# Kernel optimization log

Measured on AMD Instinct MI355X. Metric: run time of the kernel, lower is better.

Reference implementation:

```python
import jax, jax.numpy as jnp
import numpy as np


def setup_inputs() -> dict:
    key = jax.random.key(0)
    # [B, C=3, T, H, W] raw video clips
    batch_x = jax.random.normal(key, (16, 3, 600, 72, 72), dtype=jnp.float32)
    return {"batch_x": batch_x}


def reference(batch_x):
    # Spatial mean over H, W -> RGB traces  [B, 3, N]
    x = jnp.mean(batch_x, axis=(3, 4))
    # First left singular vector of each 3xN trace matrix.
    # torch.svd(X) reduced -> U is [3, 3]; batched over B here.
    U, _, _ = jnp.linalg.svd(x, full_matrices=False)  # U: [B, 3, 3]
    S = U[..., 0]  # [B, 3] dominant left singular vector
    # Orthogonal projection P = I - S S^T (sign of S is irrelevant)
    P = jnp.eye(3, dtype=x.dtype) - jnp.einsum('bi,bj->bij', S, S)  # [B, 3, 3]
    Y = jnp.einsum('bij,bjn->bin', P, x)  # [B, 3, N]
    # Original takes channel index 1 (green) of projected signal
    return Y[:, 1, :]  # [B, N]
```

## Files before the change

kernel.cpp:

```cpp
#include <hip/hip_runtime.h>
#include <math.h>

#define HW_ELEMS 5184
#define HW_VEC   1296
#define NT       600
#define NC       3
#define NB       16
#define NSLABS   (NB * NC * NT)
#define MEAN_GRID 2048

__global__ __launch_bounds__(256) void mean_kernel(const float* __restrict__ in,
                                                   float* __restrict__ xbar) {
    const int lane   = threadIdx.x & 63;
    const int gwave  = (blockIdx.x * 256 + threadIdx.x) >> 6;
    const int nwaves = (MEAN_GRID * 256) >> 6;

    for (int slab = gwave; slab < NSLABS; slab += nwaves) {
        const float4* __restrict__ p =
            (const float4*)(in + (size_t)slab * HW_ELEMS);

        float s0 = 0.f, s1 = 0.f;
        #pragma unroll
        for (int i = 0; i < 20; i += 2) {
            float4 a = p[(i << 6) + lane];
            float4 b = p[((i + 1) << 6) + lane];
            s0 += (a.x + a.y) + (a.z + a.w);
            s1 += (b.x + b.y) + (b.z + b.w);
        }
        if (lane < 16) {
            float4 v = p[1280 + lane];
            s0 += (v.x + v.y) + (v.z + v.w);
        }
        float s = s0 + s1;

        #pragma unroll
        for (int off = 32; off; off >>= 1)
            s += __shfl_xor(s, off, 64);

        if (lane == 0) xbar[slab] = s * (1.0f / (float)HW_ELEMS);
    }
}

__global__ __launch_bounds__(256) void project_kernel(const float* __restrict__ xbar,
                                                      float* __restrict__ out) {
    const int b = blockIdx.x;
    __shared__ float  sx[NC][NT];
    __shared__ double red[6][256];
    __shared__ float  S[3];

    const float* xb = xbar + b * (NC * NT);
    for (int i = threadIdx.x; i < NC * NT; i += 256)
        ((float*)sx)[i] = xb[i];
    __syncthreads();

    double g0 = 0, g1 = 0, g2 = 0, g3 = 0, g4 = 0, g5 = 0;
    for (int t = threadIdx.x; t < NT; t += 256) {
        double x0 = (double)sx[0][t];
        double x1 = (double)sx[1][t];
        double x2 = (double)sx[2][t];
        g0 += x0 * x0; g1 += x0 * x1; g2 += x0 * x2;
        g3 += x1 * x1; g4 += x1 * x2; g5 += x2 * x2;
    }
    red[0][threadIdx.x] = g0; red[1][threadIdx.x] = g1; red[2][threadIdx.x] = g2;
    red[3][threadIdx.x] = g3; red[4][threadIdx.x] = g4; red[5][threadIdx.x] = g5;
    __syncthreads();
    for (int s = 128; s > 0; s >>= 1) {
        if (threadIdx.x < s) {
            #pragma unroll
            for (int k = 0; k < 6; k++)
                red[k][threadIdx.x] += red[k][threadIdx.x + s];
        }
        __syncthreads();
    }

    if (threadIdx.x == 0) {
        double M[3][3] = {{red[0][0], red[1][0], red[2][0]},
                          {red[1][0], red[3][0], red[4][0]},
                          {red[2][0], red[4][0], red[5][0]}};
        for (int it = 0; it < 40; it++) {
            double tr = M[0][0] + M[1][1] + M[2][2];
            double inv = (tr > 0.0) ? (1.0 / tr) : 1.0;
            double T[3][3];
            #pragma unroll
            for (int i = 0; i < 3; i++)
                #pragma unroll
                for (int j = 0; j < 3; j++) T[i][j] = M[i][j] * inv;
            #pragma unroll
            for (int i = 0; i < 3; i++)
                #pragma unroll
                for (int j = 0; j < 3; j++) {
                    double acc = 0.0;
                    #pragma unroll
                    for (int k = 0; k < 3; k++) acc += T[i][k] * T[k][j];
                    M[i][j] = acc;
                }
        }
        int jm = 0;
        if (M[1][1] > M[jm][jm]) jm = 1;
        if (M[2][2] > M[jm][jm]) jm = 2;
        double v0 = M[0][jm], v1 = M[1][jm], v2 = M[2][jm];
        double nrm = sqrt(v0 * v0 + v1 * v1 + v2 * v2);
        double inv = (nrm > 0.0) ? (1.0 / nrm) : 0.0;
        S[0] = (float)(v0 * inv);
        S[1] = (float)(v1 * inv);
        S[2] = (float)(v2 * inv);
    }
    __syncthreads();

    const float s0 = S[0], s1 = S[1], s2 = S[2];
    for (int t = threadIdx.x; t < NT; t += 256) {
        float x0 = sx[0][t], x1 = sx[1][t], x2 = sx[2][t];
        float d = s0 * x0 + s1 * x1 + s2 * x2;
        out[b * NT + t] = x1 - s1 * d;
    }
}

extern "C" void kernel_launch(void* const* d_in, const int* in_sizes, int n_in,
                              void* d_out, int out_size, void* d_ws, size_t ws_size,
                              hipStream_t stream) {
    const float* batch_x = (const float*)d_in[0];
    float* out  = (float*)d_out;
    float* xbar = (float*)d_ws;

    mean_kernel<<<MEAN_GRID, 256, 0, stream>>>(batch_x, xbar);
    project_kernel<<<NB, 256, 0, stream>>>(xbar, out);
}
```

Before: 752.7 us.

## Fuse mean and projection kernels via last-block atomic counter per batch

Merges the spatial-mean and projection kernels into a single launch. Each 256-thread block reduces four slabs, one per wave, using nontemporal vector loads. The last block to finish for a batch, found with a global atomic counter, computes the Gram matrix, dominant vector and projection. This removes a kernel launch and the serial tail of the small projection kernel. In exchange it adds atomics, thread fences, and a counter that must be reset for the next call.

```diff
diff --git a/kernel.cpp b/kernel.cpp
--- a/kernel.cpp
+++ b/kernel.cpp
@@ -2,48 +2,56 @@
 #include <math.h>
 
 #define HW_ELEMS 5184
-#define HW_VEC   1296
 #define NT       600
 #define NC       3
 #define NB       16
 #define NSLABS   (NB * NC * NT)
-#define MEAN_GRID 2048
+#define SLABS_PER_BLOCK 4
+#define NBLOCKS  (NSLABS / SLABS_PER_BLOCK)
+#define BLOCKS_PER_BATCH (NBLOCKS / NB)
 
-__global__ __launch_bounds__(256) void mean_kernel(const float* __restrict__ in,
-                                                   float* __restrict__ xbar) {
-    const int lane   = threadIdx.x & 63;
-    const int gwave  = (blockIdx.x * 256 + threadIdx.x) >> 6;
-    const int nwaves = (MEAN_GRID * 256) >> 6;
+typedef float f4 __attribute__((ext_vector_type(4)));
 
-    for (int slab = gwave; slab < NSLABS; slab += nwaves) {
-        const float4* __restrict__ p =
-            (const float4*)(in + (size_t)slab * HW_ELEMS);
+__device__ unsigned int g_cnt[NB];
 
-        float s0 = 0.f, s1 = 0.f;
-        #pragma unroll
-        for (int i = 0; i < 20; i += 2) {
-            float4 a = p[(i << 6) + lane];
-            float4 b = p[((i + 1) << 6) + lane];
-            s0 += (a.x + a.y) + (a.z + a.w);
-            s1 += (b.x + b.y) + (b.z + b.w);
-        }
-        if (lane < 16) {
-            float4 v = p[1280 + lane];
-            s0 += (v.x + v.y) + (v.z + v.w);
-        }
-        float s = s0 + s1;
+__global__ __launch_bounds__(256) void fused_kernel(const float* __restrict__ in,
+                                                    float* __restrict__ xbar,
+                                                    float* __restrict__ out) {
+    const int lane = threadIdx.x & 63;
+    const int wid  = threadIdx.x >> 6;
+    const int slab = blockIdx.x * SLABS_PER_BLOCK + wid;
+    const int b    = blockIdx.x / BLOCKS_PER_BATCH;
 
-        #pragma unroll
-        for (int off = 32; off; off >>= 1)
-            s += __shfl_xor(s, off, 64);
+    const f4* __restrict__ p = (const f4*)(in + (size_t)slab * HW_ELEMS);
+    float s0 = 0.f, s1 = 0.f;
+    #pragma unroll
+    for (int i = 0; i < 20; i += 2) {
+        f4 a = __builtin_nontemporal_load(p + (i << 6) + lane);
+        f4 c = __builtin_nontemporal_load(p + ((i + 1) << 6) + lane);
+        s0 += (a.x + a.y) + (a.z + a.w);
+        s1 += (c.x + c.y) + (c.z + c.w);
+    }
+    if (lane < 16) {
+        f4 v = __builtin_nontemporal_load(p + 1280 + lane);
+        s0 += (v.x + v.y) + (v.z + v.w);
+    }
+    float s = s0 + s1;
+    #pragma unroll
+    for (int off = 32; off; off >>= 1)
+        s += __shfl_xor(s, off, 64);
+    if (lane == 0) xbar[slab] = s * (1.0f / (float)HW_ELEMS);
 
-        if (lane == 0) xbar[slab] = s * (1.0f / (float)HW_ELEMS);
+    __shared__ int is_last;
+    __syncthreads();
+    if (threadIdx.x == 0) {
+        __threadfence();
+        unsigned int old = atomicAdd(&g_cnt[b], 1u);
+        is_last = (old == BLOCKS_PER_BATCH - 1) ? 1 : 0;
     }
-}
+    __syncthreads();
+    if (!is_last) return;
+    __threadfence();
 
-__global__ __launch_bounds__(256) void project_kernel(const float* __restrict__ xbar,
-                                                      float* __restrict__ out) {
-    const int b = blockIdx.x;
     __shared__ float  sx[NC][NT];
     __shared__ double red[6][256];
     __shared__ float  S[3];
@@ -64,11 +72,11 @@
     red[0][threadIdx.x] = g0; red[1][threadIdx.x] = g1; red[2][threadIdx.x] = g2;
     red[3][threadIdx.x] = g3; red[4][threadIdx.x] = g4; red[5][threadIdx.x] = g5;
     __syncthreads();
-    for (int s = 128; s > 0; s >>= 1) {
-        if (threadIdx.x < s) {
+    for (int st = 128; st > 0; st >>= 1) {
+        if (threadIdx.x < st) {
             #pragma unroll
             for (int k = 0; k < 6; k++)
-                red[k][threadIdx.x] += red[k][threadIdx.x + s];
+                red[k][threadIdx.x] += red[k][threadIdx.x + st];
         }
         __syncthreads();
     }
@@ -107,12 +115,14 @@
     }
     __syncthreads();
 
-    const float s0 = S[0], s1 = S[1], s2 = S[2];
+    const float c0 = S[0], c1 = S[1], c2 = S[2];
     for (int t = threadIdx.x; t < NT; t += 256) {
         float x0 = sx[0][t], x1 = sx[1][t], x2 = sx[2][t];
-        float d = s0 * x0 + s1 * x1 + s2 * x2;
-        out[b * NT + t] = x1 - s1 * d;
+        float d = c0 * x0 + c1 * x1 + c2 * x2;
+        out[b * NT + t] = x1 - c1 * d;
     }
+
+    if (threadIdx.x == 0) g_cnt[b] = 0;
 }
 
 extern "C" void kernel_launch(void* const* d_in, const int* in_sizes, int n_in,
@@ -122,6 +132,5 @@
     float* out  = (float*)d_out;
     float* xbar = (float*)d_ws;
 
-    mean_kernel<<<MEAN_GRID, 256, 0, stream>>>(batch_x, xbar);
-    project_kernel<<<NB, 256, 0, stream>>>(xbar, out);
+    fused_kernel<<<NBLOCKS, 256, 0, stream>>>(batch_x, xbar, out);
 }
```

Result: slower. 1.104 ms (+46.7%).
